# Kernel optimization log

Measured on AMD Instinct MI355X. Metric: run time of the kernel, lower is better.

The kernel has to match this reference:

```python
import jax, jax.numpy as jnp
import numpy as np

T = 100000  # context_window
H = 256     # hidden_dim


def setup_inputs() -> dict:
    key = jax.random.key(0)
    k1, k2, k3, k4, k5 = jax.random.split(key, 5)
    inputs = jax.random.normal(k1, (T, H), dtype=jnp.float32)
    hc = jax.random.normal(k2, (1, H), dtype=jnp.float32)
    # learned params (original inits Wm/V to ones; random values give a better numeric test)
    Wm = jax.random.normal(k3, (H, H), dtype=jnp.float32) * (1.0 / np.sqrt(H))
    V = jax.random.normal(k4, (H, 1), dtype=jnp.float32) * (1.0 / np.sqrt(H))
    W1 = jax.random.normal(k5, (H, H), dtype=jnp.float32) * (1.0 / np.sqrt(H))
    return {"inputs": inputs, "hc": hc, "Wm": Wm, "V": V, "W1": W1}


def reference(inputs, hc, Wm, V, W1):
    # Mt: (T, H); broadcast-add the projected context vector to every row
    Mt = inputs
    proj_hc = hc @ W1.T                      # (1, H), torch Linear: x @ W^T
    At = jnp.tanh(Mt @ Wm + proj_hc) @ V     # (T, 1)
    alphat = jax.nn.log_softmax(At.reshape(1, -1), axis=1)  # (1, T)
    ct = alphat @ Mt                         # (1, H) — weighted sum with LOG-softmax weights (faithful)
    return (alphat, ct)
```

## Files before the change

kernel.cpp:

```cpp
#include <hip/hip_runtime.h>
#include <math.h>

#define T_N 100000
#define H_N 256
#define NT16 (T_N / 16)
#define NB_AT 256
#define NWAVES (NB_AT * 12)

typedef __attribute__((ext_vector_type(8))) __bf16 bf16x8;
typedef __attribute__((ext_vector_type(4))) float f32x4;


__device__ __forceinline__ float tanh_fast(float x) {
    float e = __expf(2.0f * x);
    return 1.0f - 2.0f / (e + 1.0f);
}

__global__ __launch_bounds__(256) void k_prep(const float* __restrict__ Wm,
                                              const float* __restrict__ hc,
                                              const float* __restrict__ W1,
                                              __bf16* __restrict__ WmT,
                                              float* __restrict__ proj,
                                              float* __restrict__ s1g,
                                              float* __restrict__ s0g) {
    const int j = blockIdx.x;
    const int t = threadIdx.x;
    WmT[j * H_N + t] = (__bf16)Wm[t * H_N + j];
    __shared__ float red[H_N];
    red[t] = hc[t] * W1[j * H_N + t];
    __syncthreads();
    for (int off = 128; off > 0; off >>= 1) {
        if (t < off) red[t] += red[t + off];
        __syncthreads();
    }
    if (t == 0) proj[j] = red[0];
    if (j == 0) { s1g[t] = 0.0f; s0g[t] = 0.0f; }
}

__global__ __launch_bounds__(768, 3) void k_at(const float* __restrict__ Mt,
                                               const __bf16* __restrict__ WmT,
                                               const float* __restrict__ proj,
                                               const float* __restrict__ V,
                                               float* __restrict__ At,
                                               float2* __restrict__ part2,
                                               float* __restrict__ s1g,
                                               float* __restrict__ s0g) {
    const int tid = threadIdx.x;
    const int lane = tid & 63;
    const int w = tid >> 6;
    const int l15 = lane & 15;
    const int lg = lane >> 4;

    struct SMem {
        __align__(16) char sB[131072];
        float pj[256];
        float vj[256];
        float lsem[12], lses[12];
    };
    __shared__ SMem sm;

    for (int g = tid; g < 8192; g += 768) {
        const int n = g >> 5;
        const int c = g & 31;
        const bf16x8 v = *(const bf16x8*)(WmT + n * H_N + c * 8);
        *(bf16x8*)(&sm.sB[(n * 512 + c * 16) ^ ((n & 7) << 4)]) = v;
    }
    if (tid < 256) { sm.pj[tid] = proj[tid]; sm.vj[tid] = V[tid]; }
    __syncthreads();

    const int gw = blockIdx.x * 12 + w;
    float lm = -1e30f, ls = 0.0f;
    float s1a[4] = {0.f, 0.f, 0.f, 0.f};
    float s0a[4] = {0.f, 0.f, 0.f, 0.f};

    float4 R[16];
    auto loadA = [&](int tile) {
        const int tt = (tile < NT16) ? tile : (NT16 - 1);
        const float* arow = Mt + (size_t)(tt * 16 + l15) * H_N;
#pragma unroll
        for (int ks = 0; ks < 8; ++ks) {
            R[2 * ks]     = *(const float4*)(arow + 32 * ks + 8 * lg);
            R[2 * ks + 1] = *(const float4*)(arow + 32 * ks + 8 * lg + 4);
        }
    };

    loadA(gw);

    for (int tile = gw; tile < NT16; tile += NWAVES) {
        bf16x8 af[8];
#pragma unroll
        for (int ks = 0; ks < 8; ++ks) {
            const float4 a0 = R[2 * ks], a1 = R[2 * ks + 1];
            af[ks][0] = (__bf16)a0.x; af[ks][1] = (__bf16)a0.y;
            af[ks][2] = (__bf16)a0.z; af[ks][3] = (__bf16)a0.w;
            af[ks][4] = (__bf16)a1.x; af[ks][5] = (__bf16)a1.y;
            af[ks][6] = (__bf16)a1.z; af[ks][7] = (__bf16)a1.w;
        }

        const float* crow = Mt + (size_t)tile * 16 * H_N + lane * 4;
        float4 x[16];
#pragma unroll
        for (int r = 0; r < 16; ++r)
            x[r] = *(const float4*)(crow + (size_t)r * H_N);

        float pacc[4] = {0.f, 0.f, 0.f, 0.f};
#pragma unroll 2
        for (int jb = 0; jb < 16; ++jb) {
            f32x4 accA = {0.f, 0.f, 0.f, 0.f};
            f32x4 accB = {0.f, 0.f, 0.f, 0.f};
            const int n = 16 * jb + l15;
            const int nb = n * 512;
            const int nswz = (n & 7) << 4;
#pragma unroll
            for (int ks = 0; ks < 4; ++ks) {
                const bf16x8 bfA = *(const bf16x8*)(
                    &sm.sB[nb + (((32 * ks + 8 * lg) * 2) ^ nswz)]);
                const bf16x8 bfB = *(const bf16x8*)(
                    &sm.sB[nb + (((32 * (ks + 4) + 8 * lg) * 2) ^ nswz)]);
                accA = __builtin_amdgcn_mfma_f32_16x16x32_bf16(af[ks], bfA, accA, 0, 0, 0);
                accB = __builtin_amdgcn_mfma_f32_16x16x32_bf16(af[ks + 4], bfB, accB, 0, 0, 0);
            }
            const float pjv = sm.pj[n], vjv = sm.vj[n];
#pragma unroll
            for (int i = 0; i < 4; ++i)
                pacc[i] += tanh_fast(accA[i] + accB[i] + pjv) * vjv;
        }

        float p[4];
#pragma unroll
        for (int i = 0; i < 4; ++i) {
            float q = pacc[i];
            q += __shfl_xor(q, 1);
            q += __shfl_xor(q, 2);
            q += __shfl_xor(q, 4);
            q += __shfl_xor(q, 8);
            p[i] = q;
        }
        if (l15 == 0) {
#pragma unroll
            for (int i = 0; i < 4; ++i) {
                const float at = p[i];
                At[tile * 16 + 4 * lg + i] = at;
                if (at > lm) { ls = ls * __expf(lm - at) + 1.0f; lm = at; }
                else ls += __expf(at - lm);
            }
        }

        loadA(tile + NWAVES);

#pragma unroll
        for (int r = 0; r < 16; ++r) {
            const float atr = __shfl(p[r & 3], 16 * (r >> 2));
            s1a[0] += atr * x[r].x; s1a[1] += atr * x[r].y;
            s1a[2] += atr * x[r].z; s1a[3] += atr * x[r].w;
            s0a[0] += x[r].x; s0a[1] += x[r].y;
            s0a[2] += x[r].z; s0a[3] += x[r].w;
        }
    }

#pragma unroll
    for (int d = 1; d < 64; d <<= 1) {
        const float m2 = __shfl_xor(lm, d), s2 = __shfl_xor(ls, d);
        const float M = fmaxf(lm, m2);
        ls = ls * __expf(lm - M) + s2 * __expf(m2 - M);
        lm = M;
    }
    if (lane == 0) { sm.lsem[w] = lm; sm.lses[w] = ls; }

    __syncthreads();
    float* red1 = (float*)&sm.sB[0];
    float* red2 = (float*)&sm.sB[16384];
#pragma unroll
    for (int q = 0; q < 4; ++q) {
        red1[w * 256 + lane * 4 + q] = s1a[q];
        red2[w * 256 + lane * 4 + q] = s0a[q];
    }
    __syncthreads();
    if (tid < 256) {
        float a = 0.f;
#pragma unroll
        for (int g = 0; g < 12; ++g) a += red1[g * 256 + tid];
        atomicAdd(&s1g[tid], a);
    } else if (tid < 512) {
        const int c = tid - 256;
        float a = 0.f;
#pragma unroll
        for (int g = 0; g < 12; ++g) a += red2[g * 256 + c];
        atomicAdd(&s0g[c], a);
    } else if (tid == 512) {
        float m = sm.lsem[0], s = sm.lses[0];
#pragma unroll
        for (int g = 1; g < 12; ++g) {
            const float m2 = sm.lsem[g], s2 = sm.lses[g];
            const float M = fmaxf(m, m2);
            s = s * __expf(m - M) + s2 * __expf(m2 - M);
            m = M;
        }
        part2[blockIdx.x] = make_float2(m, s);
    }
}

__global__ __launch_bounds__(256) void k_final(const float2* __restrict__ part2,
                                               const float* __restrict__ s1g,
                                               const float* __restrict__ s0g,
                                               float* __restrict__ lse,
                                               float* __restrict__ out) {
    const int tid = threadIdx.x;
    __shared__ float ms[256], ss[256];
    const float2 p = part2[tid];
    ms[tid] = p.x; ss[tid] = p.y;
    __syncthreads();
    for (int off = 128; off > 0; off >>= 1) {
        if (tid < off) {
            const float m2 = ms[tid + off], s2 = ss[tid + off];
            const float M = fmaxf(ms[tid], m2);
            ss[tid] = ss[tid] * __expf(ms[tid] - M) + s2 * __expf(m2 - M);
            ms[tid] = M;
        }
        __syncthreads();
    }
    __shared__ float Ls;
    if (tid == 0) { Ls = ms[0] + logf(ss[0]); *lse = Ls; }
    __syncthreads();
    out[T_N + tid] = s1g[tid] - Ls * s0g[tid];
}

__global__ __launch_bounds__(256) void k_alpha(const float* __restrict__ At,
                                               const float* __restrict__ lse,
                                               float* __restrict__ out) {
    const float L = *lse;
    const int i4 = blockIdx.x * 256 + threadIdx.x;
    if (i4 < T_N / 4) {
        float4 a = *(const float4*)(At + i4 * 4);
        a.x -= L; a.y -= L; a.z -= L; a.w -= L;
        *(float4*)(out + i4 * 4) = a;
    }
}

extern "C" void kernel_launch(void* const* d_in, const int* in_sizes, int n_in,
                              void* d_out, int out_size, void* d_ws, size_t ws_size,
                              hipStream_t stream) {
    const float* inputs = (const float*)d_in[0];
    const float* hc     = (const float*)d_in[1];
    const float* Wm     = (const float*)d_in[2];
    const float* V      = (const float*)d_in[3];
    const float* W1     = (const float*)d_in[4];
    float* out = (float*)d_out;

    char* ws = (char*)d_ws;
    __bf16* WmT  = (__bf16*)ws;
    float* proj  = (float*)(ws + 131072);
    float* At    = (float*)(ws + 132096);
    float2* p2   = (float2*)(ws + 532096);
    float* s1g   = (float*)(ws + 536192);
    float* s0g   = (float*)(ws + 537216);
    float* lse   = (float*)(ws + 538240);

    k_prep<<<256, 256, 0, stream>>>(Wm, hc, W1, WmT, proj, s1g, s0g);
    k_at<<<NB_AT, 768, 0, stream>>>(inputs, WmT, proj, V, At, p2, s1g, s0g);
    k_final<<<1, 256, 0, stream>>>(p2, s1g, s0g, lse, out);
    k_alpha<<<98, 256, 0, stream>>>(At, lse, out);
}
```

Baseline: 59.57 us.

## Raise k_at to 16 waves per block and drop register prefetch of A tiles

Grows the attention-score kernel from 12 to 16 waves per block and removes the software prefetch of the next tile's A fragment. The x rows are now loaded in two halves of 8, and tiles are interleaved across blocks (w*NB_AT+blockIdx). Together these cut register pressure so more waves fit per CU, relying on that extra occupancy to hide global-load latency in place of explicit prefetch. The risk is exposed load latency if occupancy does not actually rise, and the larger reduction buffers now need red2 moved further into shared memory.

```diff
diff --git a/kernel.cpp b/kernel.cpp
--- a/kernel.cpp
+++ b/kernel.cpp
@@ -5,7 +5,9 @@
 #define H_N 256
 #define NT16 (T_N / 16)
 #define NB_AT 256
-#define NWAVES (NB_AT * 12)
+#define WPB 16
+#define NTHR (WPB * 64)
+#define NWAVES (NB_AT * WPB)
 
 typedef __attribute__((ext_vector_type(8))) __bf16 bf16x8;
 typedef __attribute__((ext_vector_type(4))) float f32x4;
@@ -37,14 +39,14 @@
     if (j == 0) { s1g[t] = 0.0f; s0g[t] = 0.0f; }
 }
 
-__global__ __launch_bounds__(768, 3) void k_at(const float* __restrict__ Mt,
-                                               const __bf16* __restrict__ WmT,
-                                               const float* __restrict__ proj,
-                                               const float* __restrict__ V,
-                                               float* __restrict__ At,
-                                               float2* __restrict__ part2,
-                                               float* __restrict__ s1g,
-                                               float* __restrict__ s0g) {
+__global__ __launch_bounds__(NTHR, 4) void k_at(const float* __restrict__ Mt,
+                                                const __bf16* __restrict__ WmT,
+                                                const float* __restrict__ proj,
+                                                const float* __restrict__ V,
+                                                float* __restrict__ At,
+                                                float2* __restrict__ part2,
+                                                float* __restrict__ s1g,
+                                                float* __restrict__ s0g) {
     const int tid = threadIdx.x;
     const int lane = tid & 63;
     const int w = tid >> 6;
@@ -55,11 +57,11 @@
         __align__(16) char sB[131072];
         float pj[256];
         float vj[256];
-        float lsem[12], lses[12];
+        float lsem[WPB], lses[WPB];
     };
     __shared__ SMem sm;
 
-    for (int g = tid; g < 8192; g += 768) {
+    for (int g = tid; g < 8192; g += NTHR) {
         const int n = g >> 5;
         const int c = g & 31;
         const bf16x8 v = *(const bf16x8*)(WmT + n * H_N + c * 8);
@@ -68,40 +70,29 @@
     if (tid < 256) { sm.pj[tid] = proj[tid]; sm.vj[tid] = V[tid]; }
     __syncthreads();
 
-    const int gw = blockIdx.x * 12 + w;
     float lm = -1e30f, ls = 0.0f;
     float s1a[4] = {0.f, 0.f, 0.f, 0.f};
     float s0a[4] = {0.f, 0.f, 0.f, 0.f};
 
-    float4 R[16];
-    auto loadA = [&](int tile) {
-        const int tt = (tile < NT16) ? tile : (NT16 - 1);
-        const float* arow = Mt + (size_t)(tt * 16 + l15) * H_N;
+    for (int tile = w * NB_AT + blockIdx.x; tile < NT16; tile += NWAVES) {
+        const float* arow = Mt + (size_t)(tile * 16 + l15) * H_N;
+        const float* crow = Mt + (size_t)tile * 16 * H_N + lane * 4;
+
+        bf16x8 af[8];
 #pragma unroll
         for (int ks = 0; ks < 8; ++ks) {
-            R[2 * ks]     = *(const float4*)(arow + 32 * ks + 8 * lg);
-            R[2 * ks + 1] = *(const float4*)(arow + 32 * ks + 8 * lg + 4);
-        }
-    };
-
-    loadA(gw);
-
-    for (int tile = gw; tile < NT16; tile += NWAVES) {
-        bf16x8 af[8];
-#pragma unroll
-        for (int ks = 0; ks < 8; ++ks) {
-            const float4 a0 = R[2 * ks], a1 = R[2 * ks + 1];
+            const float4 a0 = *(const float4*)(arow + 32 * ks + 8 * lg);
+            const float4 a1 = *(const float4*)(arow + 32 * ks + 8 * lg + 4);
             af[ks][0] = (__bf16)a0.x; af[ks][1] = (__bf16)a0.y;
             af[ks][2] = (__bf16)a0.z; af[ks][3] = (__bf16)a0.w;
             af[ks][4] = (__bf16)a1.x; af[ks][5] = (__bf16)a1.y;
             af[ks][6] = (__bf16)a1.z; af[ks][7] = (__bf16)a1.w;
         }
 
-        const float* crow = Mt + (size_t)tile * 16 * H_N + lane * 4;
-        float4 x[16];
-#pragma unroll
-        for (int r = 0; r < 16; ++r)
-            x[r] = *(const float4*)(crow + (size_t)r * H_N);
+        float4 x0[8];
+#pragma unroll
+        for (int r = 0; r < 8; ++r)
+            x0[r] = *(const float4*)(crow + (size_t)r * H_N);
 
         float pacc[4] = {0.f, 0.f, 0.f, 0.f};
 #pragma unroll 2
@@ -146,15 +137,26 @@
             }
         }
 
-        loadA(tile + NWAVES);
-
-#pragma unroll
-        for (int r = 0; r < 16; ++r) {
+        float4 x1[8];
+#pragma unroll
+        for (int r = 0; r < 8; ++r)
+            x1[r] = *(const float4*)(crow + (size_t)(8 + r) * H_N);
+
+#pragma unroll
+        for (int r = 0; r < 8; ++r) {
             const float atr = __shfl(p[r & 3], 16 * (r >> 2));
-            s1a[0] += atr * x[r].x; s1a[1] += atr * x[r].y;
-            s1a[2] += atr * x[r].z; s1a[3] += atr * x[r].w;
-            s0a[0] += x[r].x; s0a[1] += x[r].y;
-            s0a[2] += x[r].z; s0a[3] += x[r].w;
+            s1a[0] += atr * x0[r].x; s1a[1] += atr * x0[r].y;
+            s1a[2] += atr * x0[r].z; s1a[3] += atr * x0[r].w;
+            s0a[0] += x0[r].x; s0a[1] += x0[r].y;
+            s0a[2] += x0[r].z; s0a[3] += x0[r].w;
+        }
+#pragma unroll
+        for (int r = 8; r < 16; ++r) {
+            const float atr = __shfl(p[r & 3], 16 * (r >> 2));
+            s1a[0] += atr * x1[r - 8].x; s1a[1] += atr * x1[r - 8].y;
+            s1a[2] += atr * x1[r - 8].z; s1a[3] += atr * x1[r - 8].w;
+            s0a[0] += x1[r - 8].x; s0a[1] += x1[r - 8].y;
+            s0a[2] += x1[r - 8].z; s0a[3] += x1[r - 8].w;
         }
     }
 
@@ -169,7 +171,7 @@
 
     __syncthreads();
     float* red1 = (float*)&sm.sB[0];
-    float* red2 = (float*)&sm.sB[16384];
+    float* red2 = (float*)&sm.sB[65536];
 #pragma unroll
     for (int q = 0; q < 4; ++q) {
         red1[w * 256 + lane * 4 + q] = s1a[q];
@@ -179,18 +181,18 @@
     if (tid < 256) {
         float a = 0.f;
 #pragma unroll
-        for (int g = 0; g < 12; ++g) a += red1[g * 256 + tid];
+        for (int g = 0; g < WPB; ++g) a += red1[g * 256 + tid];
         atomicAdd(&s1g[tid], a);
     } else if (tid < 512) {
         const int c = tid - 256;
         float a = 0.f;
 #pragma unroll
-        for (int g = 0; g < 12; ++g) a += red2[g * 256 + c];
+        for (int g = 0; g < WPB; ++g) a += red2[g * 256 + c];
         atomicAdd(&s0g[c], a);
     } else if (tid == 512) {
         float m = sm.lsem[0], s = sm.lses[0];
 #pragma unroll
-        for (int g = 1; g < 12; ++g) {
+        for (int g = 1; g < WPB; ++g) {
             const float m2 = sm.lsem[g], s2 = sm.lses[g];
             const float M = fmaxf(m, m2);
             s = s * __expf(m - M) + s2 * __expf(m2 - M);
@@ -257,7 +259,7 @@
     float* lse   = (float*)(ws + 538240);
 
     k_prep<<<256, 256, 0, stream>>>(Wm, hc, W1, WmT, proj, s1g, s0g);
-    k_at<<<NB_AT, 768, 0, stream>>>(inputs, WmT, proj, V, At, p2, s1g, s0g);
+    k_at<<<NB_AT, NTHR, 0, stream>>>(inputs, WmT, proj, V, At, p2, s1g, s0g);
     k_final<<<1, 256, 0, stream>>>(p2, s1g, s0g, lse, out);
     k_alpha<<<98, 256, 0, stream>>>(At, lse, out);
 }
```

New measurement: 57.61 us (median of 2 runs). 1.03x faster.

## Use atomic work-stealing tile scheduler and defer weighted-sum accumulation

Applied to the files above, without the earlier changes.

Replaces the static strided tile assignment with a global atomic counter from which each wave grabs its next 16-row tile, so the load can balance across waves. The A-fragment register prefetch is removed. Instead, the weighted-sum accumulation for the previous tile is deferred until after the next tile's A load is issued, which keeps some overlap. This adds a global atomic and a shuffle per tile and loses the explicit next-tile prefetch. The red2 offset also moves to avoid overlap with red1.

```diff
diff --git a/kernel.cpp b/kernel.cpp
--- a/kernel.cpp
+++ b/kernel.cpp
@@ -5,7 +5,8 @@
 #define H_N 256
 #define NT16 (T_N / 16)
 #define NB_AT 256
-#define NWAVES (NB_AT * 12)
+#define WPB 12
+#define NTHR (WPB * 64)
 
 typedef __attribute__((ext_vector_type(8))) __bf16 bf16x8;
 typedef __attribute__((ext_vector_type(4))) float f32x4;
@@ -22,7 +23,8 @@
                                               __bf16* __restrict__ WmT,
                                               float* __restrict__ proj,
                                               float* __restrict__ s1g,
-                                              float* __restrict__ s0g) {
+                                              float* __restrict__ s0g,
+                                              int* __restrict__ cnt) {
     const int j = blockIdx.x;
     const int t = threadIdx.x;
     WmT[j * H_N + t] = (__bf16)Wm[t * H_N + j];
@@ -35,16 +37,18 @@
     }
     if (t == 0) proj[j] = red[0];
     if (j == 0) { s1g[t] = 0.0f; s0g[t] = 0.0f; }
-}
-
-__global__ __launch_bounds__(768, 3) void k_at(const float* __restrict__ Mt,
-                                               const __bf16* __restrict__ WmT,
-                                               const float* __restrict__ proj,
-                                               const float* __restrict__ V,
-                                               float* __restrict__ At,
-                                               float2* __restrict__ part2,
-                                               float* __restrict__ s1g,
-                                               float* __restrict__ s0g) {
+    if (j == 0 && t == 0) *cnt = 0;
+}
+
+__global__ __launch_bounds__(NTHR, 3) void k_at(const float* __restrict__ Mt,
+                                                const __bf16* __restrict__ WmT,
+                                                const float* __restrict__ proj,
+                                                const float* __restrict__ V,
+                                                float* __restrict__ At,
+                                                float2* __restrict__ part2,
+                                                float* __restrict__ s1g,
+                                                float* __restrict__ s0g,
+                                                int* __restrict__ cnt) {
     const int tid = threadIdx.x;
     const int lane = tid & 63;
     const int w = tid >> 6;
@@ -55,11 +59,11 @@
         __align__(16) char sB[131072];
         float pj[256];
         float vj[256];
-        float lsem[12], lses[12];
+        float lsem[WPB], lses[WPB];
     };
     __shared__ SMem sm;
 
-    for (int g = tid; g < 8192; g += 768) {
+    for (int g = tid; g < 8192; g += NTHR) {
         const int n = g >> 5;
         const int c = g & 31;
         const bf16x8 v = *(const bf16x8*)(WmT + n * H_N + c * 8);
@@ -68,37 +72,47 @@
     if (tid < 256) { sm.pj[tid] = proj[tid]; sm.vj[tid] = V[tid]; }
     __syncthreads();
 
-    const int gw = blockIdx.x * 12 + w;
     float lm = -1e30f, ls = 0.0f;
     float s1a[4] = {0.f, 0.f, 0.f, 0.f};
     float s0a[4] = {0.f, 0.f, 0.f, 0.f};
 
-    float4 R[16];
-    auto loadA = [&](int tile) {
-        const int tt = (tile < NT16) ? tile : (NT16 - 1);
-        const float* arow = Mt + (size_t)(tt * 16 + l15) * H_N;
+    auto grab = [&]() -> int {
+        int t;
+        if (lane == 0) t = atomicAdd(cnt, 1);
+        return __shfl(t, 0);
+    };
+
+    float4 x[16];
+    float pprev[4];
+    int have_prev = 0;
+
+    int t = grab();
+    while (t < NT16) {
+        const float* arow = Mt + (size_t)(t * 16 + l15) * H_N;
+        const float* crow = Mt + (size_t)t * 16 * H_N + lane * 4;
+
+        bf16x8 af[8];
 #pragma unroll
         for (int ks = 0; ks < 8; ++ks) {
-            R[2 * ks]     = *(const float4*)(arow + 32 * ks + 8 * lg);
-            R[2 * ks + 1] = *(const float4*)(arow + 32 * ks + 8 * lg + 4);
-        }
-    };
-
-    loadA(gw);
-
-    for (int tile = gw; tile < NT16; tile += NWAVES) {
-        bf16x8 af[8];
-#pragma unroll
-        for (int ks = 0; ks < 8; ++ks) {
-            const float4 a0 = R[2 * ks], a1 = R[2 * ks + 1];
+            const float4 a0 = *(const float4*)(arow + 32 * ks + 8 * lg);
+            const float4 a1 = *(const float4*)(arow + 32 * ks + 8 * lg + 4);
             af[ks][0] = (__bf16)a0.x; af[ks][1] = (__bf16)a0.y;
             af[ks][2] = (__bf16)a0.z; af[ks][3] = (__bf16)a0.w;
             af[ks][4] = (__bf16)a1.x; af[ks][5] = (__bf16)a1.y;
             af[ks][6] = (__bf16)a1.z; af[ks][7] = (__bf16)a1.w;
         }
 
-        const float* crow = Mt + (size_t)tile * 16 * H_N + lane * 4;
-        float4 x[16];
+        if (have_prev) {
+#pragma unroll
+            for (int r = 0; r < 16; ++r) {
+                const float atr = __shfl(pprev[r & 3], 16 * (r >> 2));
+                s1a[0] += atr * x[r].x; s1a[1] += atr * x[r].y;
+                s1a[2] += atr * x[r].z; s1a[3] += atr * x[r].w;
+                s0a[0] += x[r].x; s0a[1] += x[r].y;
+                s0a[2] += x[r].z; s0a[3] += x[r].w;
+            }
+        }
+
 #pragma unroll
         for (int r = 0; r < 16; ++r)
             x[r] = *(const float4*)(crow + (size_t)r * H_N);
@@ -126,7 +140,6 @@
                 pacc[i] += tanh_fast(accA[i] + accB[i] + pjv) * vjv;
         }
 
-        float p[4];
 #pragma unroll
         for (int i = 0; i < 4; ++i) {
             float q = pacc[i];
@@ -134,23 +147,25 @@
             q += __shfl_xor(q, 2);
             q += __shfl_xor(q, 4);
             q += __shfl_xor(q, 8);
-            p[i] = q;
+            pprev[i] = q;
         }
         if (l15 == 0) {
 #pragma unroll
             for (int i = 0; i < 4; ++i) {
-                const float at = p[i];
-                At[tile * 16 + 4 * lg + i] = at;
+                const float at = pprev[i];
+                At[t * 16 + 4 * lg + i] = at;
                 if (at > lm) { ls = ls * __expf(lm - at) + 1.0f; lm = at; }
                 else ls += __expf(at - lm);
             }
         }
-
-        loadA(tile + NWAVES);
-
+        have_prev = 1;
+        t = grab();
+    }
+
+    if (have_prev) {
 #pragma unroll
         for (int r = 0; r < 16; ++r) {
-            const float atr = __shfl(p[r & 3], 16 * (r >> 2));
+            const float atr = __shfl(pprev[r & 3], 16 * (r >> 2));
             s1a[0] += atr * x[r].x; s1a[1] += atr * x[r].y;
             s1a[2] += atr * x[r].z; s1a[3] += atr * x[r].w;
             s0a[0] += x[r].x; s0a[1] += x[r].y;
@@ -169,7 +184,7 @@
 
     __syncthreads();
     float* red1 = (float*)&sm.sB[0];
-    float* red2 = (float*)&sm.sB[16384];
+    float* red2 = (float*)&sm.sB[65536];
 #pragma unroll
     for (int q = 0; q < 4; ++q) {
         red1[w * 256 + lane * 4 + q] = s1a[q];
@@ -179,18 +194,18 @@
     if (tid < 256) {
         float a = 0.f;
 #pragma unroll
-        for (int g = 0; g < 12; ++g) a += red1[g * 256 + tid];
+        for (int g = 0; g < WPB; ++g) a += red1[g * 256 + tid];
         atomicAdd(&s1g[tid], a);
     } else if (tid < 512) {
         const int c = tid - 256;
         float a = 0.f;
 #pragma unroll
-        for (int g = 0; g < 12; ++g) a += red2[g * 256 + c];
+        for (int g = 0; g < WPB; ++g) a += red2[g * 256 + c];
         atomicAdd(&s0g[c], a);
     } else if (tid == 512) {
         float m = sm.lsem[0], s = sm.lses[0];
 #pragma unroll
-        for (int g = 1; g < 12; ++g) {
+        for (int g = 1; g < WPB; ++g) {
             const float m2 = sm.lsem[g], s2 = sm.lses[g];
             const float M = fmaxf(m, m2);
             s = s * __expf(m - M) + s2 * __expf(m2 - M);
@@ -255,9 +270,10 @@
     float* s1g   = (float*)(ws + 536192);
     float* s0g   = (float*)(ws + 537216);
     float* lse   = (float*)(ws + 538240);
-
-    k_prep<<<256, 256, 0, stream>>>(Wm, hc, W1, WmT, proj, s1g, s0g);
-    k_at<<<NB_AT, 768, 0, stream>>>(inputs, WmT, proj, V, At, p2, s1g, s0g);
+    int* cnt     = (int*)(ws + 538244);
+
+    k_prep<<<256, 256, 0, stream>>>(Wm, hc, W1, WmT, proj, s1g, s0g, cnt);
+    k_at<<<NB_AT, NTHR, 0, stream>>>(inputs, WmT, proj, V, At, p2, s1g, s0g, cnt);
     k_final<<<1, 256, 0, stream>>>(p2, s1g, s0g, lse, out);
     k_alpha<<<98, 256, 0, stream>>>(At, lse, out);
 }
```

Result: slower. 137.8 us (+131.4%).
